# Optimization experiments

Measured on AMD Instinct MI355X. Metric: run time of the kernel, lower is better.

Reference implementation:

```python
import jax, jax.numpy as jnp
import numpy as np

WINDOW_SIZE = 11
SIGMA = 1.5
C1 = 0.01 ** 2
C2 = 0.03 ** 2


def _gaussian_window(channel, window_size=WINDOW_SIZE, sigma=SIGMA):
    # 1D gaussian, normalized, then outer product -> 2D window, replicated per channel
    x = np.arange(window_size)
    g = np.exp(-((x - window_size // 2) ** 2) / (2.0 * sigma ** 2))
    g = g / g.sum()
    w2d = np.outer(g, g).astype(np.float32)            # [K, K]
    w = np.broadcast_to(w2d, (channel, 1, window_size, window_size))  # OIHW depthwise
    return jnp.asarray(w)


def _dwconv(x, window):
    # depthwise conv2d, SAME-style padding = window//2 (matches F.conv2d padding=K//2)
    pad = WINDOW_SIZE // 2
    return jax.lax.conv_general_dilated(
        x, window,
        window_strides=(1, 1),
        padding=[(pad, pad), (pad, pad)],
        feature_group_count=x.shape[1],
        dimension_numbers=("NCHW", "OIHW", "NCHW"),
    )


def setup_inputs() -> dict:
    key = jax.random.key(0)
    k1, k2 = jax.random.split(key)
    B, C, H, W = 16, 3, 512, 512
    pred = jax.random.uniform(k1, (B, C, H, W), dtype=jnp.float32)
    gt = jax.random.uniform(k2, (B, C, H, W), dtype=jnp.float32)
    return {"pred": pred, "gt": gt}


def reference(pred, gt):
    channel = pred.shape[1]
    window = _gaussian_window(channel).astype(pred.dtype)

    mu1 = _dwconv(pred, window)
    mu2 = _dwconv(gt, window)
    mu1_sq = mu1 * mu1
    mu2_sq = mu2 * mu2
    mu1_mu2 = mu1 * mu2

    sigma1_sq = _dwconv(pred * pred, window) - mu1_sq
    sigma2_sq = _dwconv(gt * gt, window) - mu2_sq
    sigma12 = _dwconv(pred * gt, window) - mu1_mu2

    ssim_map = ((2 * mu1_mu2 + C1) * (2 * sigma12 + C2)) / (
        (mu1_sq + mu2_sq + C1) * (sigma1_sq + sigma2_sq + C2)
    )
    # size_average=True -> scalar mean; loss = 1 - ssim
    return 1.0 - jnp.mean(ssim_map)
```

## Files before the change

kernel.cpp:

```cpp
#include <hip/hip_runtime.h>

#define IMG 512
#define CS 36
#define CH_STRIDE (16 * CS)
#define WV_STRIDE (5 * CH_STRIDE)

typedef short short8  __attribute__((ext_vector_type(8)));
typedef float floatx4 __attribute__((ext_vector_type(4)));
typedef int   intx2   __attribute__((ext_vector_type(2)));

__device__ static constexpr float W11F[11] = {
    0.00102838f, 0.00759876f, 0.03600077f, 0.10936069f, 0.21300554f,
    0.26601173f,
    0.21300554f, 0.10936069f, 0.03600077f, 0.00759876f, 0.00102838f};

__device__ __forceinline__ unsigned pack2bf16(float a, float b) {
    const unsigned ua = __float_as_uint(a) + 0x8000u;
    const unsigned ub = __float_as_uint(b) + 0x8000u;
    return __builtin_amdgcn_perm(ub, ua, 0x07060302u);
}

__device__ __forceinline__ void ht_store(ushort* p, floatx4 c) {
    intx2 d;
    d.x = (int)pack2bf16(c[0], c[1]);
    d.y = (int)pack2bf16(c[2], c[3]);
    *(intx2*)p = d;
}

__device__ __forceinline__ short8 ht_load(const ushort* p) {
    union { intx2 d[2]; short8 s; } u;
    u.d[0] = *(const intx2*)p;
    u.d[1] = *(const intx2*)(p + 4);
    return u.s;
}

__global__ __launch_bounds__(256, 4) void ssim_mfma_roll(
        const float* __restrict__ pred, const float* __restrict__ gt,
        float* __restrict__ partials)
{
    __shared__ ushort Ht[4 * WV_STRIDE];
    __shared__ ushort wlut[16];
    __shared__ float wsum[4];

    const int tid  = threadIdx.x;
    const int wv   = tid >> 6;
    const int lane = tid & 63;
    const int n    = lane & 15;
    const int quad = lane >> 4;

    if (tid < 16) {
        const float w = (tid < 11) ? W11F[tid] : 0.f;
        wlut[tid] = (ushort)((__float_as_uint(w) + 0x8000u) >> 16);
    }
    __syncthreads();

    short8 band;
#pragma unroll
    for (int j = 0; j < 8; ++j) {
        const int t = quad * 8 + j - n - 3;
        band[j] = (short)wlut[((unsigned)t < 11u) ? t : 15];
    }

    const int bx = blockIdx.x, yh = blockIdx.y, plane = blockIdx.z;
    const long pb = (long)plane * (IMG * IMG);
    const float* pplane = pred + pb;
    const float* gplane = gt + pb;
    const int xs  = bx * 64 + wv * 16 - 8;
    const int y0  = yh * 256;
    ushort* ht    = &Ht[wv * WV_STRIDE];
    const bool cols_ok = (xs >= 0) && (xs + 32 <= IMG);

#define LOADT(t, pf, gf)                                                     \
    {                                                                        \
        const int ys  = y0 - 8 + (t) * 16;                                   \
        const int row = ys + n;                                              \
        const int c0  = xs + quad * 8;                                       \
        if (cols_ok && ys >= 0 && ys + 16 <= IMG) {                          \
            const float* pr = pplane + (long)row * IMG + c0;                 \
            const float* gr = gplane + (long)row * IMG + c0;                 \
            *(float4*)&pf[0] = *(const float4*)pr;                           \
            *(float4*)&pf[4] = *(const float4*)(pr + 4);                     \
            *(float4*)&gf[0] = *(const float4*)gr;                           \
            *(float4*)&gf[4] = *(const float4*)(gr + 4);                     \
        } else {                                                             \
            const bool rv = (unsigned)row < (unsigned)IMG;                   \
            const int rowc = rv ? row : 0;                                   \
            const float* pr = pplane + (long)rowc * IMG;                     \
            const float* gr = gplane + (long)rowc * IMG;                     \
            _Pragma("unroll")                                                \
            for (int j = 0; j < 8; ++j) {                                    \
                const int cc = c0 + j;                                       \
                const bool ok = rv && ((unsigned)cc < (unsigned)IMG);        \
                const int ccc = ok ? cc : 0;                                 \
                const float pv = pr[ccc], gv = gr[ccc];                      \
                pf[j] = ok ? pv : 0.f;                                       \
                gf[j] = ok ? gv : 0.f;                                       \
            }                                                                \
        }                                                                    \
    }

#define COMPT(t, pf, gf)                                                     \
    {                                                                        \
        union { unsigned u[4]; short8 s; } ap, ag, app, agg, apg;            \
        _Pragma("unroll")                                                    \
        for (int h = 0; h < 4; ++h) {                                        \
            const float p0 = pf[2*h], p1 = pf[2*h+1];                        \
            const float g0 = gf[2*h], g1 = gf[2*h+1];                        \
            ap.u [h] = pack2bf16(p0, p1);                                    \
            ag.u [h] = pack2bf16(g0, g1);                                    \
            app.u[h] = pack2bf16(p0 * p0, p1 * p1);                          \
            agg.u[h] = pack2bf16(g0 * g0, g1 * g1);                          \
            apg.u[h] = pack2bf16(p0 * g0, p1 * g1);                          \
        }                                                                    \
        const floatx4 z = {0.f, 0.f, 0.f, 0.f};                              \
        const floatx4 cp  = __builtin_amdgcn_mfma_f32_16x16x32_bf16(ap.s,  band, z, 0, 0, 0); \
        const floatx4 cg  = __builtin_amdgcn_mfma_f32_16x16x32_bf16(ag.s,  band, z, 0, 0, 0); \
        const floatx4 cpp = __builtin_amdgcn_mfma_f32_16x16x32_bf16(app.s, band, z, 0, 0, 0); \
        const floatx4 cgg = __builtin_amdgcn_mfma_f32_16x16x32_bf16(agg.s, band, z, 0, 0, 0); \
        const floatx4 cpg = __builtin_amdgcn_mfma_f32_16x16x32_bf16(apg.s, band, z, 0, 0, 0); \
        const int wb = n * CS + ((t) & 1) * 16 + quad * 4;                   \
        ht_store(&ht[0 * CH_STRIDE + wb], cp);                               \
        ht_store(&ht[1 * CH_STRIDE + wb], cg);                               \
        ht_store(&ht[2 * CH_STRIDE + wb], cpp);                              \
        ht_store(&ht[3 * CH_STRIDE + wb], cgg);                              \
        ht_store(&ht[4 * CH_STRIDE + wb], cpg);                              \
    }

#define VPASS(SLO, SHI)                                                      \
    {                                                                        \
        const int koff = ((quad < 2) ? (SLO) : (SHI)) * 16 + (quad & 1) * 8; \
        const int rb   = n * CS + koff;                                      \
        const short8 bp  = ht_load(&ht[0 * CH_STRIDE + rb]);                 \
        const short8 bg  = ht_load(&ht[1 * CH_STRIDE + rb]);                 \
        const short8 bpp = ht_load(&ht[2 * CH_STRIDE + rb]);                 \
        const short8 bgg = ht_load(&ht[3 * CH_STRIDE + rb]);                 \
        const short8 bpg = ht_load(&ht[4 * CH_STRIDE + rb]);                 \
        const floatx4 z = {0.f, 0.f, 0.f, 0.f};                              \
        const floatx4 mp  = __builtin_amdgcn_mfma_f32_16x16x32_bf16(band, bp,  z, 0, 0, 0); \
        const floatx4 mg  = __builtin_amdgcn_mfma_f32_16x16x32_bf16(band, bg,  z, 0, 0, 0); \
        const floatx4 mpp = __builtin_amdgcn_mfma_f32_16x16x32_bf16(band, bpp, z, 0, 0, 0); \
        const floatx4 mgg = __builtin_amdgcn_mfma_f32_16x16x32_bf16(band, bgg, z, 0, 0, 0); \
        const floatx4 mpg = __builtin_amdgcn_mfma_f32_16x16x32_bf16(band, bpg, z, 0, 0, 0); \
        _Pragma("unroll")                                                    \
        for (int r = 0; r < 4; ++r) {                                        \
            const float mu1 = mp[r], mu2 = mg[r];                            \
            const float mu1sq = mu1 * mu1, mu2sq = mu2 * mu2;                \
            const float mu12 = mu1 * mu2;                                    \
            const float s1  = mpp[r] - mu1sq;                                \
            const float s2  = mgg[r] - mu2sq;                                \
            const float s12 = mpg[r] - mu12;                                 \
            const float num = (2.f * mu12 + C1) * (2.f * s12 + C2);          \
            const float den = (mu1sq + mu2sq + C1) * (s1 + s2 + C2);         \
            lsum += num * __builtin_amdgcn_rcpf(den);                        \
        }                                                                    \
    }

    const float C1 = 1e-4f, C2 = 9e-4f;
    float lsum = 0.f;

    float pA[8], gA[8], pB[8], gB[8];

    LOADT(0, pA, gA)
    LOADT(1, pB, gB)
    COMPT(0, pA, gA)
    LOADT(2, pA, gA)
    COMPT(1, pB, gB)
    VPASS(0, 1)

    for (int t = 2; t <= 14; t += 2) {
        LOADT(t + 1, pB, gB)
        COMPT(t, pA, gA)
        VPASS(1, 0)
        LOADT(t + 2, pA, gA)
        COMPT(t + 1, pB, gB)
        VPASS(0, 1)
    }

    COMPT(16, pA, gA)
    VPASS(1, 0)

#pragma unroll
    for (int off = 32; off > 0; off >>= 1)
        lsum += __shfl_down(lsum, off);
    if (lane == 0) wsum[wv] = lsum;
    __syncthreads();
    if (tid == 0)
        partials[(plane * 2 + yh) * 8 + bx] =
            wsum[0] + wsum[1] + wsum[2] + wsum[3];
}

__global__ __launch_bounds__(1024) void ssim_finalize(
        const float* __restrict__ partials, float* __restrict__ out,
        int nparts, double inv_n)
{
    __shared__ double ws[16];
    double s = 0.0;
    for (int i = threadIdx.x; i < nparts; i += 1024)
        s += (double)partials[i];
#pragma unroll
    for (int off = 32; off > 0; off >>= 1)
        s += __shfl_down(s, off);
    if ((threadIdx.x & 63) == 0) ws[threadIdx.x >> 6] = s;
    __syncthreads();
    if (threadIdx.x == 0) {
        double t = 0.0;
#pragma unroll
        for (int i = 0; i < 16; ++i) t += ws[i];
        out[0] = (float)(1.0 - t * inv_n);
    }
}

extern "C" void kernel_launch(void* const* d_in, const int* in_sizes, int n_in,
                              void* d_out, int out_size, void* d_ws, size_t ws_size,
                              hipStream_t stream)
{
    const float* pred = (const float*)d_in[0];
    const float* gt   = (const float*)d_in[1];
    float* out        = (float*)d_out;
    float* partials   = (float*)d_ws;

    const long n = (long)in_sizes[0];
    const int planes = (int)(n / (long)(IMG * IMG));

    dim3 grid(8, 2, planes);
    ssim_mfma_roll<<<grid, 256, 0, stream>>>(pred, gt, partials);
    ssim_finalize<<<1, 1024, 0, stream>>>(partials, out,
                                          8 * 2 * planes, 1.0 / (double)n);
}
```

Baseline: 161.1 us.

## Stream input tiles via async global-to-LDS DMA with triple buffering per wave

Replaces register-staged global loads with global_load_lds transfers into a triple-buffered, XOR-swizzled LDS staging area. Explicit vmcnt waits and sched barriers pipeline three tiles ahead. Out-of-bounds rows and columns are clamped during the copy and then zeroed in LDS afterwards. The block shrinks to a single 64-thread wave with a 4x larger grid, which drops the cross-wave reduction and __syncthreads. This aims to hide global memory latency better, at the cost of relying on hand-coded waitcnt encodings and on the FIX zeroing being ordered correctly with the DMA.

```diff
diff --git a/kernel.cpp b/kernel.cpp
--- a/kernel.cpp
+++ b/kernel.cpp
@@ -34,23 +34,21 @@
     return u.s;
 }
 
-__global__ __launch_bounds__(256, 4) void ssim_mfma_roll(
+__global__ __launch_bounds__(64) void ssim_mfma_dma(
         const float* __restrict__ pred, const float* __restrict__ gt,
         float* __restrict__ partials)
 {
-    __shared__ ushort Ht[4 * WV_STRIDE];
+    __shared__ __align__(16) ushort Ht[WV_STRIDE];
+    __shared__ __align__(16) float  Sst[3][2][512];
     __shared__ ushort wlut[16];
-    __shared__ float wsum[4];
-
-    const int tid  = threadIdx.x;
-    const int wv   = tid >> 6;
-    const int lane = tid & 63;
+
+    const int lane = threadIdx.x;
     const int n    = lane & 15;
     const int quad = lane >> 4;
 
-    if (tid < 16) {
-        const float w = (tid < 11) ? W11F[tid] : 0.f;
-        wlut[tid] = (ushort)((__float_as_uint(w) + 0x8000u) >> 16);
+    if (lane < 16) {
+        const float w = (lane < 11) ? W11F[lane] : 0.f;
+        wlut[lane] = (ushort)((__float_as_uint(w) + 0x8000u) >> 16);
     }
     __syncthreads();
 
@@ -65,37 +63,49 @@
     const long pb = (long)plane * (IMG * IMG);
     const float* pplane = pred + pb;
     const float* gplane = gt + pb;
-    const int xs  = bx * 64 + wv * 16 - 8;
-    const int y0  = yh * 256;
-    ushort* ht    = &Ht[wv * WV_STRIDE];
-    const bool cols_ok = (xs >= 0) && (xs + 32 <= IMG);
-
-#define LOADT(t, pf, gf)                                                     \
-    {                                                                        \
-        const int ys  = y0 - 8 + (t) * 16;                                   \
-        const int row = ys + n;                                              \
-        const int c0  = xs + quad * 8;                                       \
-        if (cols_ok && ys >= 0 && ys + 16 <= IMG) {                          \
-            const float* pr = pplane + (long)row * IMG + c0;                 \
-            const float* gr = gplane + (long)row * IMG + c0;                 \
-            *(float4*)&pf[0] = *(const float4*)pr;                           \
-            *(float4*)&pf[4] = *(const float4*)(pr + 4);                     \
-            *(float4*)&gf[0] = *(const float4*)gr;                           \
-            *(float4*)&gf[4] = *(const float4*)(gr + 4);                     \
-        } else {                                                             \
-            const bool rv = (unsigned)row < (unsigned)IMG;                   \
-            const int rowc = rv ? row : 0;                                   \
-            const float* pr = pplane + (long)rowc * IMG;                     \
-            const float* gr = gplane + (long)rowc * IMG;                     \
-            _Pragma("unroll")                                                \
-            for (int j = 0; j < 8; ++j) {                                    \
-                const int cc = c0 + j;                                       \
-                const bool ok = rv && ((unsigned)cc < (unsigned)IMG);        \
-                const int ccc = ok ? cc : 0;                                 \
-                const float pv = pr[ccc], gv = gr[ccc];                      \
-                pf[j] = ok ? pv : 0.f;                                       \
-                gf[j] = ok ? gv : 0.f;                                       \
-            }                                                                \
+    const int xs = bx * 16 - 8;
+    const int y0 = yh * 256;
+    ushort* ht   = &Ht[0];
+
+    const int lr   = lane >> 3;
+    const int pos  = lane & 7;
+    const int sch  = pos ^ (lr & 7);
+    const int c0s  = xs + sch * 4;
+    const bool colOOB = (c0s < 0) || (c0s > IMG - 4);
+    const int scol = colOOB ? 0 : c0s;
+
+#define AS1 const __attribute__((address_space(1))) void*
+#define AS3 __attribute__((address_space(3))) void*
+
+#define STAGE(t, b)                                                          \
+    {                                                                        \
+        const int ys_ = y0 - 8 + (t) * 16;                                   \
+        int ra = ys_ + lr;                                                   \
+        int rb = ys_ + lr + 8;                                               \
+        ra = ra < 0 ? 0 : (ra > IMG - 1 ? IMG - 1 : ra);                     \
+        rb = rb < 0 ? 0 : (rb > IMG - 1 ? IMG - 1 : rb);                     \
+        const float* pa_ = pplane + (long)ra * IMG + scol;                   \
+        const float* pb_ = pplane + (long)rb * IMG + scol;                   \
+        const float* ga_ = gplane + (long)ra * IMG + scol;                   \
+        const float* gb_ = gplane + (long)rb * IMG + scol;                   \
+        __builtin_amdgcn_global_load_lds((AS1)pa_, (AS3)&Sst[b][0][0],   16, 0, 0); \
+        __builtin_amdgcn_global_load_lds((AS1)pb_, (AS3)&Sst[b][0][256], 16, 0, 0); \
+        __builtin_amdgcn_global_load_lds((AS1)ga_, (AS3)&Sst[b][1][0],   16, 0, 0); \
+        __builtin_amdgcn_global_load_lds((AS1)gb_, (AS3)&Sst[b][1][256], 16, 0, 0); \
+    }
+
+#define FIX(t, b)                                                            \
+    {                                                                        \
+        const int ys_ = y0 - 8 + (t) * 16;                                   \
+        const int ra = ys_ + lr, rb = ra + 8;                                \
+        const float4 f4z = {0.f, 0.f, 0.f, 0.f};                             \
+        if (colOOB || ((unsigned)ra > (unsigned)(IMG - 1))) {                \
+            *(float4*)&Sst[b][0][lane * 4] = f4z;                            \
+            *(float4*)&Sst[b][1][lane * 4] = f4z;                            \
+        }                                                                    \
+        if (colOOB || ((unsigned)rb > (unsigned)(IMG - 1))) {                \
+            *(float4*)&Sst[b][0][256 + lane * 4] = f4z;                      \
+            *(float4*)&Sst[b][1][256 + lane * 4] = f4z;                      \
         }                                                                    \
     }
 
@@ -124,6 +134,19 @@
         ht_store(&ht[2 * CH_STRIDE + wb], cpp);                              \
         ht_store(&ht[3 * CH_STRIDE + wb], cgg);                              \
         ht_store(&ht[4 * CH_STRIDE + wb], cpg);                              \
+    }
+
+#define COMPL(t, b)                                                          \
+    {                                                                        \
+        const int sw8_ = n & 7;                                              \
+        const int o0 = n * 32 + ((((quad << 1))     ^ sw8_) << 2);           \
+        const int o1 = n * 32 + ((((quad << 1) | 1) ^ sw8_) << 2);           \
+        float pf[8], gf[8];                                                  \
+        *(float4*)&pf[0] = *(const float4*)&Sst[b][0][o0];                   \
+        *(float4*)&pf[4] = *(const float4*)&Sst[b][0][o1];                   \
+        *(float4*)&gf[0] = *(const float4*)&Sst[b][1][o0];                   \
+        *(float4*)&gf[4] = *(const float4*)&Sst[b][1][o1];                   \
+        COMPT(t, pf, gf)                                                     \
     }
 
 #define VPASS(SLO, SHI)                                                      \
@@ -155,38 +178,41 @@
         }                                                                    \
     }
 
+#define WAITV8 { __builtin_amdgcn_s_waitcnt(0x0F78); __builtin_amdgcn_sched_barrier(0); }
+#define WAITV4 { __builtin_amdgcn_s_waitcnt(0x0F74); __builtin_amdgcn_sched_barrier(0); }
+#define WAITV0 { __builtin_amdgcn_s_waitcnt(0x0F70); __builtin_amdgcn_sched_barrier(0); }
+#define SBAR __builtin_amdgcn_sched_barrier(0);
+
     const float C1 = 1e-4f, C2 = 9e-4f;
     float lsum = 0.f;
 
-    float pA[8], gA[8], pB[8], gB[8];
-
-    LOADT(0, pA, gA)
-    LOADT(1, pB, gB)
-    COMPT(0, pA, gA)
-    LOADT(2, pA, gA)
-    COMPT(1, pB, gB)
-    VPASS(0, 1)
-
-    for (int t = 2; t <= 14; t += 2) {
-        LOADT(t + 1, pB, gB)
-        COMPT(t, pA, gA)
-        VPASS(1, 0)
-        LOADT(t + 2, pA, gA)
-        COMPT(t + 1, pB, gB)
-        VPASS(0, 1)
-    }
-
-    COMPT(16, pA, gA)
-    VPASS(1, 0)
+    STAGE(0, 0)
+    STAGE(1, 1)
+    STAGE(2, 2)
+
+    WAITV8 FIX(0, 0) COMPL(0, 0) SBAR STAGE(3, 0)
+    WAITV8 FIX(1, 1) COMPL(1, 1) SBAR STAGE(4, 1) VPASS(0, 1)
+
+#pragma unroll
+    for (int t = 2; t <= 13; ++t) {
+        const int b = t % 3;
+        WAITV8
+        FIX(t, b)
+        COMPL(t, b)
+        SBAR
+        STAGE(t + 3, b)
+        VPASS((t - 1) & 1, t & 1)
+    }
+
+    WAITV8 FIX(14, 2) COMPL(14, 2) VPASS(1, 0)
+    WAITV4 FIX(15, 0) COMPL(15, 0) VPASS(0, 1)
+    WAITV0 FIX(16, 1) COMPL(16, 1) VPASS(1, 0)
 
 #pragma unroll
     for (int off = 32; off > 0; off >>= 1)
         lsum += __shfl_down(lsum, off);
-    if (lane == 0) wsum[wv] = lsum;
-    __syncthreads();
-    if (tid == 0)
-        partials[(plane * 2 + yh) * 8 + bx] =
-            wsum[0] + wsum[1] + wsum[2] + wsum[3];
+    if (lane == 0)
+        partials[(plane * 2 + yh) * 32 + bx] = lsum;
 }
 
 __global__ __launch_bounds__(1024) void ssim_finalize(
@@ -222,8 +248,8 @@
     const long n = (long)in_sizes[0];
     const int planes = (int)(n / (long)(IMG * IMG));
 
-    dim3 grid(8, 2, planes);
-    ssim_mfma_roll<<<grid, 256, 0, stream>>>(pred, gt, partials);
+    dim3 grid(32, 2, planes);
+    ssim_mfma_dma<<<grid, 64, 0, stream>>>(pred, gt, partials);
     ssim_finalize<<<1, 1024, 0, stream>>>(partials, out,
-                                          8 * 2 * planes, 1.0 / (double)n);
-}
+                                          32 * 2 * planes, 1.0 / (double)n);
+}
```

Measured after the change: 159.8 us. Within noise of the previous version (-0.9%).

## Process two column strips per wave with shorter vertical runs

Applied to the files above, without the earlier changes.

Each wave now handles two independent 16-column strips, interleaving their loads, horizontal MFMA passes and vertical passes. Blocks cover 128 columns by 128 rows instead of 64 by 256, so the grid becomes 4x4 per plane. The aim is more independent work per wave to hide memory and MFMA latency. The cost is more vertical halo overhead from the shorter row runs (9 tiles for 8 outputs), double the LDS footprint and higher register pressure.

```diff
diff --git a/kernel.cpp b/kernel.cpp
--- a/kernel.cpp
+++ b/kernel.cpp
@@ -34,11 +34,11 @@
     return u.s;
 }
 
-__global__ __launch_bounds__(256, 4) void ssim_mfma_roll(
+__global__ __launch_bounds__(256, 4) void ssim_mfma_dual(
         const float* __restrict__ pred, const float* __restrict__ gt,
         float* __restrict__ partials)
 {
-    __shared__ ushort Ht[4 * WV_STRIDE];
+    __shared__ ushort Ht[8 * WV_STRIDE];
     __shared__ ushort wlut[16];
     __shared__ float wsum[4];
 
@@ -65,17 +65,20 @@
     const long pb = (long)plane * (IMG * IMG);
     const float* pplane = pred + pb;
     const float* gplane = gt + pb;
-    const int xs  = bx * 64 + wv * 16 - 8;
-    const int y0  = yh * 256;
-    ushort* ht    = &Ht[wv * WV_STRIDE];
-    const bool cols_ok = (xs >= 0) && (xs + 32 <= IMG);
-
-#define LOADT(t, pf, gf)                                                     \
+    const int y0  = yh * 128;
+    const int xs0 = bx * 128 + wv * 16 - 8;
+    const int xs1 = xs0 + 64;
+    ushort* ht0   = &Ht[(wv * 2 + 0) * WV_STRIDE];
+    ushort* ht1   = &Ht[(wv * 2 + 1) * WV_STRIDE];
+    const bool cok0 = (xs0 >= 0) && (xs0 + 32 <= IMG);
+    const bool cok1 = (xs1 >= 0) && (xs1 + 32 <= IMG);
+
+#define LOADT(t, pf, gf, XS, COK)                                            \
     {                                                                        \
         const int ys  = y0 - 8 + (t) * 16;                                   \
         const int row = ys + n;                                              \
-        const int c0  = xs + quad * 8;                                       \
-        if (cols_ok && ys >= 0 && ys + 16 <= IMG) {                          \
+        const int c0  = (XS) + quad * 8;                                     \
+        if ((COK) && ys >= 0 && ys + 16 <= IMG) {                            \
             const float* pr = pplane + (long)row * IMG + c0;                 \
             const float* gr = gplane + (long)row * IMG + c0;                 \
             *(float4*)&pf[0] = *(const float4*)pr;                           \
@@ -99,7 +102,7 @@
         }                                                                    \
     }
 
-#define COMPT(t, pf, gf)                                                     \
+#define COMPT(t, pf, gf, HT)                                                 \
     {                                                                        \
         union { unsigned u[4]; short8 s; } ap, ag, app, agg, apg;            \
         _Pragma("unroll")                                                    \
@@ -119,22 +122,22 @@
         const floatx4 cgg = __builtin_amdgcn_mfma_f32_16x16x32_bf16(agg.s, band, z, 0, 0, 0); \
         const floatx4 cpg = __builtin_amdgcn_mfma_f32_16x16x32_bf16(apg.s, band, z, 0, 0, 0); \
         const int wb = n * CS + ((t) & 1) * 16 + quad * 4;                   \
-        ht_store(&ht[0 * CH_STRIDE + wb], cp);                               \
-        ht_store(&ht[1 * CH_STRIDE + wb], cg);                               \
-        ht_store(&ht[2 * CH_STRIDE + wb], cpp);                              \
-        ht_store(&ht[3 * CH_STRIDE + wb], cgg);                              \
-        ht_store(&ht[4 * CH_STRIDE + wb], cpg);                              \
-    }
-
-#define VPASS(SLO, SHI)                                                      \
+        ht_store(&(HT)[0 * CH_STRIDE + wb], cp);                             \
+        ht_store(&(HT)[1 * CH_STRIDE + wb], cg);                             \
+        ht_store(&(HT)[2 * CH_STRIDE + wb], cpp);                            \
+        ht_store(&(HT)[3 * CH_STRIDE + wb], cgg);                            \
+        ht_store(&(HT)[4 * CH_STRIDE + wb], cpg);                            \
+    }
+
+#define VPASS(SLO, SHI, HT)                                                  \
     {                                                                        \
         const int koff = ((quad < 2) ? (SLO) : (SHI)) * 16 + (quad & 1) * 8; \
         const int rb   = n * CS + koff;                                      \
-        const short8 bp  = ht_load(&ht[0 * CH_STRIDE + rb]);                 \
-        const short8 bg  = ht_load(&ht[1 * CH_STRIDE + rb]);                 \
-        const short8 bpp = ht_load(&ht[2 * CH_STRIDE + rb]);                 \
-        const short8 bgg = ht_load(&ht[3 * CH_STRIDE + rb]);                 \
-        const short8 bpg = ht_load(&ht[4 * CH_STRIDE + rb]);                 \
+        const short8 bp  = ht_load(&(HT)[0 * CH_STRIDE + rb]);               \
+        const short8 bg  = ht_load(&(HT)[1 * CH_STRIDE + rb]);               \
+        const short8 bpp = ht_load(&(HT)[2 * CH_STRIDE + rb]);               \
+        const short8 bgg = ht_load(&(HT)[3 * CH_STRIDE + rb]);               \
+        const short8 bpg = ht_load(&(HT)[4 * CH_STRIDE + rb]);               \
         const floatx4 z = {0.f, 0.f, 0.f, 0.f};                              \
         const floatx4 mp  = __builtin_amdgcn_mfma_f32_16x16x32_bf16(band, bp,  z, 0, 0, 0); \
         const floatx4 mg  = __builtin_amdgcn_mfma_f32_16x16x32_bf16(band, bg,  z, 0, 0, 0); \
@@ -158,26 +161,27 @@
     const float C1 = 1e-4f, C2 = 9e-4f;
     float lsum = 0.f;
 
-    float pA[8], gA[8], pB[8], gB[8];
-
-    LOADT(0, pA, gA)
-    LOADT(1, pB, gB)
-    COMPT(0, pA, gA)
-    LOADT(2, pA, gA)
-    COMPT(1, pB, gB)
-    VPASS(0, 1)
-
-    for (int t = 2; t <= 14; t += 2) {
-        LOADT(t + 1, pB, gB)
-        COMPT(t, pA, gA)
-        VPASS(1, 0)
-        LOADT(t + 2, pA, gA)
-        COMPT(t + 1, pB, gB)
-        VPASS(0, 1)
-    }
-
-    COMPT(16, pA, gA)
-    VPASS(1, 0)
+    float pA0[8], gA0[8], pB0[8], gB0[8];
+    float pA1[8], gA1[8], pB1[8], gB1[8];
+
+    LOADT(0, pA0, gA0, xs0, cok0) LOADT(0, pA1, gA1, xs1, cok1)
+    LOADT(1, pB0, gB0, xs0, cok0) LOADT(1, pB1, gB1, xs1, cok1)
+    COMPT(0, pA0, gA0, ht0)       COMPT(0, pA1, gA1, ht1)
+    LOADT(2, pA0, gA0, xs0, cok0) LOADT(2, pA1, gA1, xs1, cok1)
+    COMPT(1, pB0, gB0, ht0)       COMPT(1, pB1, gB1, ht1)
+    VPASS(0, 1, ht0)              VPASS(0, 1, ht1)
+
+    for (int t = 2; t <= 6; t += 2) {
+        LOADT(t + 1, pB0, gB0, xs0, cok0) LOADT(t + 1, pB1, gB1, xs1, cok1)
+        COMPT(t, pA0, gA0, ht0)           COMPT(t, pA1, gA1, ht1)
+        VPASS(1, 0, ht0)                  VPASS(1, 0, ht1)
+        LOADT(t + 2, pA0, gA0, xs0, cok0) LOADT(t + 2, pA1, gA1, xs1, cok1)
+        COMPT(t + 1, pB0, gB0, ht0)       COMPT(t + 1, pB1, gB1, ht1)
+        VPASS(0, 1, ht0)                  VPASS(0, 1, ht1)
+    }
+
+    COMPT(8, pA0, gA0, ht0) COMPT(8, pA1, gA1, ht1)
+    VPASS(1, 0, ht0)        VPASS(1, 0, ht1)
 
 #pragma unroll
     for (int off = 32; off > 0; off >>= 1)
@@ -185,7 +189,7 @@
     if (lane == 0) wsum[wv] = lsum;
     __syncthreads();
     if (tid == 0)
-        partials[(plane * 2 + yh) * 8 + bx] =
+        partials[(plane * 4 + yh) * 4 + bx] =
             wsum[0] + wsum[1] + wsum[2] + wsum[3];
 }
 
@@ -222,8 +226,8 @@
     const long n = (long)in_sizes[0];
     const int planes = (int)(n / (long)(IMG * IMG));
 
-    dim3 grid(8, 2, planes);
-    ssim_mfma_roll<<<grid, 256, 0, stream>>>(pred, gt, partials);
+    dim3 grid(4, 4, planes);
+    ssim_mfma_dual<<<grid, 256, 0, stream>>>(pred, gt, partials);
     ssim_finalize<<<1, 1024, 0, stream>>>(partials, out,
-                                          8 * 2 * planes, 1.0 / (double)n);
-}
+                                          4 * 4 * planes, 1.0 / (double)n);
+}
```

After: 162.2 us. About the same (+0.7%).

## Replace LDS transpose between MFMA passes with register permlane swaps

Applied to the files above, without the earlier changes.

The horizontal-pass MFMA results are no longer written to shared memory and read back for the vertical pass. They are packed to bf16 in registers and rearranged across lanes with permlane32/permlane16 swap builtins to form the B fragments directly. This removes LDS traffic, the LDS footprint and the associated waits. In exchange it adds cross-lane permute instructions and register pressure, and the occupancy hint in launch bounds is dropped.

```diff
diff --git a/kernel.cpp b/kernel.cpp
--- a/kernel.cpp
+++ b/kernel.cpp
@@ -1,13 +1,10 @@
 #include <hip/hip_runtime.h>
 
 #define IMG 512
-#define CS 36
-#define CH_STRIDE (16 * CS)
-#define WV_STRIDE (5 * CH_STRIDE)
 
 typedef short short8  __attribute__((ext_vector_type(8)));
 typedef float floatx4 __attribute__((ext_vector_type(4)));
-typedef int   intx2   __attribute__((ext_vector_type(2)));
+typedef unsigned uvec2 __attribute__((ext_vector_type(2)));
 
 __device__ static constexpr float W11F[11] = {
     0.00102838f, 0.00759876f, 0.03600077f, 0.10936069f, 0.21300554f,
@@ -20,25 +17,10 @@
     return __builtin_amdgcn_perm(ub, ua, 0x07060302u);
 }
 
-__device__ __forceinline__ void ht_store(ushort* p, floatx4 c) {
-    intx2 d;
-    d.x = (int)pack2bf16(c[0], c[1]);
-    d.y = (int)pack2bf16(c[2], c[3]);
-    *(intx2*)p = d;
-}
-
-__device__ __forceinline__ short8 ht_load(const ushort* p) {
-    union { intx2 d[2]; short8 s; } u;
-    u.d[0] = *(const intx2*)p;
-    u.d[1] = *(const intx2*)(p + 4);
-    return u.s;
-}
-
-__global__ __launch_bounds__(256, 4) void ssim_mfma_roll(
+__global__ __launch_bounds__(256) void ssim_mfma_reg(
         const float* __restrict__ pred, const float* __restrict__ gt,
         float* __restrict__ partials)
 {
-    __shared__ ushort Ht[4 * WV_STRIDE];
     __shared__ ushort wlut[16];
     __shared__ float wsum[4];
 
@@ -67,7 +49,6 @@
     const float* gplane = gt + pb;
     const int xs  = bx * 64 + wv * 16 - 8;
     const int y0  = yh * 256;
-    ushort* ht    = &Ht[wv * WV_STRIDE];
     const bool cols_ok = (xs >= 0) && (xs + 32 <= IMG);
 
 #define LOADT(t, pf, gf)                                                     \
@@ -99,7 +80,7 @@
         }                                                                    \
     }
 
-#define COMPT(t, pf, gf)                                                     \
+#define COMPH(pf, gf, PK)                                                    \
     {                                                                        \
         union { unsigned u[4]; short8 s; } ap, ag, app, agg, apg;            \
         _Pragma("unroll")                                                    \
@@ -118,23 +99,36 @@
         const floatx4 cpp = __builtin_amdgcn_mfma_f32_16x16x32_bf16(app.s, band, z, 0, 0, 0); \
         const floatx4 cgg = __builtin_amdgcn_mfma_f32_16x16x32_bf16(agg.s, band, z, 0, 0, 0); \
         const floatx4 cpg = __builtin_amdgcn_mfma_f32_16x16x32_bf16(apg.s, band, z, 0, 0, 0); \
-        const int wb = n * CS + ((t) & 1) * 16 + quad * 4;                   \
-        ht_store(&ht[0 * CH_STRIDE + wb], cp);                               \
-        ht_store(&ht[1 * CH_STRIDE + wb], cg);                               \
-        ht_store(&ht[2 * CH_STRIDE + wb], cpp);                              \
-        ht_store(&ht[3 * CH_STRIDE + wb], cgg);                              \
-        ht_store(&ht[4 * CH_STRIDE + wb], cpg);                              \
-    }
-
-#define VPASS(SLO, SHI)                                                      \
-    {                                                                        \
-        const int koff = ((quad < 2) ? (SLO) : (SHI)) * 16 + (quad & 1) * 8; \
-        const int rb   = n * CS + koff;                                      \
-        const short8 bp  = ht_load(&ht[0 * CH_STRIDE + rb]);                 \
-        const short8 bg  = ht_load(&ht[1 * CH_STRIDE + rb]);                 \
-        const short8 bpp = ht_load(&ht[2 * CH_STRIDE + rb]);                 \
-        const short8 bgg = ht_load(&ht[3 * CH_STRIDE + rb]);                 \
-        const short8 bpg = ht_load(&ht[4 * CH_STRIDE + rb]);                 \
+        PK[0] = pack2bf16(cp [0], cp [1]); PK[1] = pack2bf16(cp [2], cp [3]); \
+        PK[2] = pack2bf16(cg [0], cg [1]); PK[3] = pack2bf16(cg [2], cg [3]); \
+        PK[4] = pack2bf16(cpp[0], cpp[1]); PK[5] = pack2bf16(cpp[2], cpp[3]); \
+        PK[6] = pack2bf16(cgg[0], cgg[1]); PK[7] = pack2bf16(cgg[2], cgg[3]); \
+        PK[8] = pack2bf16(cpg[0], cpg[1]); PK[9] = pack2bf16(cpg[2], cpg[3]); \
+    }
+
+#define BFRAG(PLO, PHI, q, OUT)                                              \
+    short8 OUT;                                                              \
+    {                                                                        \
+        const uvec2 s0 = __builtin_amdgcn_permlane32_swap(                   \
+            PLO[2*(q)],     PHI[2*(q)],     false, false);                   \
+        const uvec2 t0 = __builtin_amdgcn_permlane16_swap(                   \
+            s0[0], s0[1], false, false);                                     \
+        const uvec2 s1 = __builtin_amdgcn_permlane32_swap(                   \
+            PLO[2*(q)+1],   PHI[2*(q)+1],   false, false);                   \
+        const uvec2 t1 = __builtin_amdgcn_permlane16_swap(                   \
+            s1[0], s1[1], false, false);                                     \
+        union { unsigned u[4]; short8 s; } b_;                               \
+        b_.u[0] = t0[0]; b_.u[1] = t1[0]; b_.u[2] = t0[1]; b_.u[3] = t1[1];  \
+        OUT = b_.s;                                                          \
+    }
+
+#define VWIN(PLO, PHI)                                                       \
+    {                                                                        \
+        BFRAG(PLO, PHI, 0, bp)                                               \
+        BFRAG(PLO, PHI, 1, bg)                                               \
+        BFRAG(PLO, PHI, 2, bpp)                                              \
+        BFRAG(PLO, PHI, 3, bgg)                                              \
+        BFRAG(PLO, PHI, 4, bpg)                                              \
         const floatx4 z = {0.f, 0.f, 0.f, 0.f};                              \
         const floatx4 mp  = __builtin_amdgcn_mfma_f32_16x16x32_bf16(band, bp,  z, 0, 0, 0); \
         const floatx4 mg  = __builtin_amdgcn_mfma_f32_16x16x32_bf16(band, bg,  z, 0, 0, 0); \
@@ -159,25 +153,26 @@
     float lsum = 0.f;
 
     float pA[8], gA[8], pB[8], gB[8];
+    unsigned PKE[10], PKO[10];
 
     LOADT(0, pA, gA)
     LOADT(1, pB, gB)
-    COMPT(0, pA, gA)
+    COMPH(pA, gA, PKE)
     LOADT(2, pA, gA)
-    COMPT(1, pB, gB)
-    VPASS(0, 1)
+    COMPH(pB, gB, PKO)
+    VWIN(PKE, PKO)
 
     for (int t = 2; t <= 14; t += 2) {
         LOADT(t + 1, pB, gB)
-        COMPT(t, pA, gA)
-        VPASS(1, 0)
+        COMPH(pA, gA, PKE)
+        VWIN(PKO, PKE)
         LOADT(t + 2, pA, gA)
-        COMPT(t + 1, pB, gB)
-        VPASS(0, 1)
-    }
-
-    COMPT(16, pA, gA)
-    VPASS(1, 0)
+        COMPH(pB, gB, PKO)
+        VWIN(PKE, PKO)
+    }
+
+    COMPH(pA, gA, PKE)
+    VWIN(PKO, PKE)
 
 #pragma unroll
     for (int off = 32; off > 0; off >>= 1)
@@ -223,7 +218,7 @@
     const int planes = (int)(n / (long)(IMG * IMG));
 
     dim3 grid(8, 2, planes);
-    ssim_mfma_roll<<<grid, 256, 0, stream>>>(pred, gt, partials);
+    ssim_mfma_reg<<<grid, 256, 0, stream>>>(pred, gt, partials);
     ssim_finalize<<<1, 1024, 0, stream>>>(partials, out,
                                           8 * 2 * planes, 1.0 / (double)n);
 }
```

New measurement: 154.7 us. 4.0% less time.
